# Kernel optimization log

Measured on AMD Instinct MI355X. Metric: run time of the kernel, lower is better.

The kernel has to match this reference:

```python
import jax, jax.numpy as jnp
import numpy as np
import math

B, IMG, P, C_IN = 32, 32, 2, 4
D, TED, L, H = 768, 256, 12, 12
GRID = IMG // P            # 16
N = GRID * GRID            # 256 patches
HD = D // H                # 64 head dim
MLP_H = 4 * D
RPD = 2 * GRID - 1         # 31 relative-position table side


def _ln(x, w, b, eps=1e-6):
    m = x.mean(-1, keepdims=True)
    v = ((x - m) ** 2).mean(-1, keepdims=True)
    return (x - m) * jax.lax.rsqrt(v + eps) * w + b


def _rel_idx():
    c = jnp.arange(GRID)
    ch, cw = jnp.meshgrid(c, c, indexing='ij')
    cf = jnp.stack([ch.reshape(-1), cw.reshape(-1)])          # [2, N]
    rel = cf[:, :, None] - cf[:, None, :] + (GRID - 1)        # [2, N, N] in [0, 2*GRID-2]
    return rel[0], rel[1]


def setup_inputs() -> dict:
    key = jax.random.key(0)
    ks = iter(jax.random.split(key, 64))
    def nrm(shape, s=0.02):
        return jax.random.normal(next(ks), shape, jnp.float32) * s
    z = lambda *s: jnp.zeros(s, jnp.float32)
    o = lambda *s: jnp.ones(s, jnp.float32)
    return dict(
        x=jax.random.normal(next(ks), (B, C_IN, IMG, IMG), jnp.float32),
        t=jax.random.uniform(next(ks), (B,), jnp.float32) * 1000.0,
        patch_w=nrm((D, C_IN, P, P), 0.5), patch_b=z(D),
        pos_embed=nrm((1, N, D)),
        t_w1=nrm((TED, D)), t_b1=z(D), t_w2=nrm((D, D)), t_b2=z(D),
        norm1_w=o(L, D), norm1_b=z(L, D),
        wqs=nrm((L, D, D)), bqs=z(L, D), wqt=nrm((L, D, D)), bqt=z(L, D),
        wks=nrm((L, D, D)), bks=z(L, D), wkt=nrm((L, D, D)), bkt=z(L, D),
        wvs=nrm((L, D, D)), bvs=z(L, D), wvt=nrm((L, D, D)), bvt=z(L, D),
        attn_proj_w=nrm((L, D, D)), attn_proj_b=z(L, D),
        rpb=nrm((L, RPD, RPD, H)),
        norm2_w=o(L, D), norm2_b=z(L, D),
        mlp_w1=nrm((L, D, MLP_H)), mlp_b1=z(L, MLP_H),
        mlp_w2=nrm((L, MLP_H, D)), mlp_b2=z(L, D),
        norm_w=o(D), norm_b=z(D),
        dec_w=nrm((D, P * P * C_IN)), dec_b=z(P * P * C_IN),
    )


def reference(x, t, patch_w, patch_b, pos_embed, t_w1, t_b1, t_w2, t_b2,
              norm1_w, norm1_b, wqs, bqs, wqt, bqt, wks, bks, wkt, bkt,
              wvs, bvs, wvt, bvt, attn_proj_w, attn_proj_b, rpb,
              norm2_w, norm2_b, mlp_w1, mlp_b1, mlp_w2, mlp_b2,
              norm_w, norm_b, dec_w, dec_b):
    Bn = x.shape[0]
    # patch embed: stride==kernel Conv2d as reshape + einsum -> [B, N, D]
    xr = x.reshape(Bn, C_IN, GRID, P, GRID, P)
    x_s = jnp.einsum('bcipjq,ecpq->bije', xr, patch_w).reshape(Bn, N, D) + patch_b
    x_s = x_s + pos_embed
    # sinusoidal time embedding + MLP -> [B, D]
    half = TED // 2
    freq = jnp.exp(jnp.arange(half, dtype=jnp.float32) * (-math.log(10000.0) / (half - 1)))
    emb = t[:, None] * freq[None, :]
    emb = jnp.concatenate([jnp.sin(emb), jnp.cos(emb)], axis=-1)
    x_t = jax.nn.silu(emb @ t_w1 + t_b1) @ t_w2 + t_b2
    ih, iw = _rel_idx()
    scale = HD ** -0.5
    for l in range(L):
        h = _ln(x_s, norm1_w[l], norm1_b[l])
        q = h @ wqs[l] + bqs[l] + (x_t @ wqt[l] + bqt[l])[:, None, :]
        k = h @ wks[l] + bks[l] + (x_t @ wkt[l] + bkt[l])[:, None, :]
        v = h @ wvs[l] + bvs[l] + (x_t @ wvt[l] + bvt[l])[:, None, :]
        q = q.reshape(Bn, N, H, HD)
        k = k.reshape(Bn, N, H, HD)
        v = v.reshape(Bn, N, H, HD)
        bias = rpb[l][ih, iw]                                  # gather: [N, N, H]
        attn = jnp.einsum('bnhd,bmhd->bhnm', q, k) * scale + bias.transpose(2, 0, 1)[None]
        attn = jax.nn.softmax(attn, axis=-1)
        o_ = jnp.einsum('bhnm,bmhd->bnhd', attn, v).reshape(Bn, N, D)
        x_s = x_s + (o_ @ attn_proj_w[l] + attn_proj_b[l])
        h2 = _ln(x_s, norm2_w[l], norm2_b[l])
        x_s = x_s + (jax.nn.silu(h2 @ mlp_w1[l] + mlp_b1[l]) @ mlp_w2[l] + mlp_b2[l])
    x_s = _ln(x_s, norm_w, norm_b)
    x_s = x_s @ dec_w + dec_b                                  # [B, N, P*P*C]
    # unpatchify -> [B, C, IMG, IMG]
    xo = x_s.reshape(Bn, GRID, GRID, C_IN, P, P).transpose(0, 3, 1, 4, 2, 5)
    return xo.reshape(Bn, C_IN, GRID * P, GRID * P)
```

## Files before the change

### kernel.cpp

```cpp
#include <hip/hip_runtime.h>
#include <hip/hip_bf16.h>

typedef __attribute__((ext_vector_type(8))) short short8;
typedef __attribute__((ext_vector_type(4))) float f32x4;
typedef __hip_bfloat16 bf16;

#define AS1 __attribute__((address_space(1)))
#define AS3 __attribute__((address_space(3)))

__device__ __forceinline__ void gld_lds16(const void* g, void* lds) {
  __builtin_amdgcn_global_load_lds((const AS1 unsigned int*)g,
                                   (AS3 unsigned int*)lds, 16, 0, 0);
}

__global__ void transpose_conv(const float* __restrict__ src, bf16* __restrict__ dst,
                               int R, int C, int row_off, long long layer_stride) {
  __shared__ float t[32][33];
  int l = blockIdx.z;
  int r0 = blockIdx.y * 32;
  int c0 = blockIdx.x * 32;
  int tx = threadIdx.x & 31, ty = threadIdx.x >> 5;
  const float* s = src + (size_t)l * R * C;
#pragma unroll
  for (int i = 0; i < 4; ++i)
    t[ty + i * 8][tx] = s[(size_t)(r0 + ty + i * 8) * C + c0 + tx];
  __syncthreads();
  bf16* d = dst + (size_t)l * layer_stride;
#pragma unroll
  for (int i = 0; i < 4; ++i) {
    int n = c0 + ty + i * 8, k = r0 + tx;
    d[(size_t)(row_off + n) * R + k] = __float2bfloat16(t[tx][ty + i * 8]);
  }
}

__global__ void dec_transpose(const float* __restrict__ dw, bf16* __restrict__ dwT) {
  int idx = blockIdx.x * 256 + threadIdx.x;
  if (idx >= 12288) return;
  int k = idx % 768, j = idx / 768;
  dwT[j * 768 + k] = __float2bfloat16(dw[k * 16 + j]);
}

__global__ void patch_embed(const float* __restrict__ x, const float* __restrict__ pw,
                            const float* __restrict__ pb, const float* __restrict__ pos,
                            float* __restrict__ xs) {
  int idx = blockIdx.x * 256 + threadIdx.x;
  int d = idx % 768;
  int n = (idx / 768) & 255;
  int b = idx / (768 * 256);
  int gi = n >> 4, gj = n & 15;
  float acc = pb[d];
#pragma unroll
  for (int c = 0; c < 4; ++c)
#pragma unroll
    for (int p = 0; p < 2; ++p)
#pragma unroll
      for (int q = 0; q < 2; ++q)
        acc += x[((b * 4 + c) * 32 + gi * 2 + p) * 32 + gj * 2 + q] *
               pw[((d * 4 + c) * 2 + p) * 2 + q];
  xs[idx] = acc + pos[n * 768 + d];
}

__global__ void temb_kernel(const float* __restrict__ t, float* __restrict__ emb) {
  int b = blockIdx.x;
  int i = threadIdx.x;
  float f = __expf((float)i * (-logf(10000.f) / 127.f));
  float e = t[b] * f;
  emb[b * 256 + i] = sinf(e);
  emb[b * 256 + 128 + i] = cosf(e);
}

template <int MODE>
__global__ void smallmm_red(const float* __restrict__ in, const float* __restrict__ w,
                            const float* __restrict__ bias, void* __restrict__ out, int K) {
  int tid = threadIdx.x;
  int s = tid & 7, o = blockIdx.x * 32 + (tid >> 3);
  int d = o % 768, b = o / 768;
  int Ks = K >> 3, k0 = s * Ks;
  const float* ir = in + b * K + k0;
  const float* wr = w + (size_t)k0 * 768 + d;
  float a = 0.f;
  for (int i = 0; i < Ks; ++i) a += ir[i] * wr[(size_t)i * 768];
  a += __shfl_xor(a, 1);
  a += __shfl_xor(a, 2);
  a += __shfl_xor(a, 4);
  if (s == 0) {
    a += bias[d];
    if (MODE == 0) {
      a = a / (1.f + __expf(-a));
      ((float*)out)[o] = a;
    } else {
      ((bf16*)out)[o] = __float2bfloat16(a);
    }
  }
}

__global__ void build_btab(const float* __restrict__ rpb, bf16* __restrict__ btab) {
  int idx = blockIdx.x * 256 + threadIdx.x;
  int k = idx & 255, q = (idx >> 8) & 255;
  int lh = idx >> 16;
  int h = lh % 12, l = lh / 12;
  int ih = (q >> 4) - (k >> 4) + 15;
  int iw = (q & 15) - (k & 15) + 15;
  btab[idx] = __float2bfloat16(rpb[((l * 31 + ih) * 31 + iw) * 12 + h]);
}

__global__ __launch_bounds__(256) void ln_bf16_kernel(const float* __restrict__ x,
                                                      const float* __restrict__ w,
                                                      const float* __restrict__ b,
                                                      bf16* __restrict__ out) {
  int row = blockIdx.x;
  int tid = threadIdx.x;
  const float* xr = x + (size_t)row * 768;
  float v[3];
  float s = 0.f, s2 = 0.f;
#pragma unroll
  for (int i = 0; i < 3; ++i) {
    v[i] = xr[tid + i * 256];
    s += v[i];
    s2 += v[i] * v[i];
  }
#pragma unroll
  for (int off = 32; off; off >>= 1) {
    s += __shfl_down(s, off);
    s2 += __shfl_down(s2, off);
  }
  __shared__ float ps[4], ps2[4];
  int wid = tid >> 6, lane = tid & 63;
  if (lane == 0) { ps[wid] = s; ps2[wid] = s2; }
  __syncthreads();
  s = ps[0] + ps[1] + ps[2] + ps[3];
  s2 = ps2[0] + ps2[1] + ps2[2] + ps2[3];
  float m = s * (1.f / 768.f);
  float var = s2 * (1.f / 768.f) - m * m;
  float r = rsqrtf(var + 1e-6f);
#pragma unroll
  for (int i = 0; i < 3; ++i) {
    int c = tid + i * 256;
    out[(size_t)row * 768 + c] = __float2bfloat16((v[i] - m) * r * w[c] + b[c]);
  }
}

template <int EPI>
__global__ __launch_bounds__(256) void gemm128(
    const bf16* __restrict__ A, int lda, const bf16* __restrict__ BT, int ldb, int K,
    const float* __restrict__ p0, const float* __restrict__ p1,
    const float* __restrict__ p2, const float* __restrict__ p3,
    const float* __restrict__ p4, const float* __restrict__ p5,
    const float* __restrict__ resid, float* __restrict__ outF,
    bf16* __restrict__ outB, int ldc) {
  __shared__ __align__(16) char lds[65536];
  const int tid = threadIdx.x;
  const int wid = tid >> 6, lane = tid & 63;
  const int wr = wid >> 1, wc = wid & 1;
  const int nwg = gridDim.x * gridDim.y;
  const int bid = blockIdx.y * gridDim.x + blockIdx.x;
  const int swzb = (bid & 7) * (nwg >> 3) + (bid >> 3);
  const int m0 = (swzb / gridDim.x) * 128, n0 = (swzb % gridDim.x) * 128;
  const int l16 = lane & 15, lq = lane >> 4;

  f32x4 acc[4][4];
#pragma unroll
  for (int i = 0; i < 4; ++i)
#pragma unroll
    for (int j = 0; j < 4; ++j) acc[i][j] = f32x4{0.f, 0.f, 0.f, 0.f};

  const int arow = tid >> 3;
  const int aslot = (tid & 7) ^ (arow & 7);
  const bf16* gA = A + (size_t)(m0 + arow) * lda + aslot * 8;
  const bf16* gB = BT + (size_t)(n0 + arow) * ldb + aslot * 8;
  const unsigned offw = (unsigned)__builtin_amdgcn_readfirstlane((tid & ~63) * 16);

  const int NT = K >> 6;
  auto stage = [&](int buf, int t) {
    char* p = lds + buf * 32768;
    const int k = t * 64;
#pragma unroll
    for (int it = 0; it < 4; ++it) {
      gld_lds16(gA + (size_t)it * 32 * lda + k, p + it * 4096 + offw);
      gld_lds16(gB + (size_t)it * 32 * ldb + k, p + 16384 + it * 4096 + offw);
    }
  };

  stage(0, 0);
  const unsigned swb = ((unsigned)(l16 & 7)) << 4;
  for (int t = 0; t < NT; ++t) {
    char* cur = lds + (t & 1) * 32768;
    if (t + 1 < NT) {
      stage((t + 1) & 1, t + 1);
      asm volatile("s_waitcnt vmcnt(8)" ::: "memory");
    } else {
      asm volatile("s_waitcnt vmcnt(0)" ::: "memory");
    }
    __builtin_amdgcn_s_barrier();
#pragma unroll
    for (int ks = 0; ks < 2; ++ks) {
      short8 af[4], bfr[4];
      const unsigned ko = ((unsigned)(ks * 64 + lq * 16)) ^ swb;
#pragma unroll
      for (int i = 0; i < 4; ++i) {
        af[i]  = *(const short8*)(cur + (wr * 64 + i * 16 + l16) * 128 + ko);
        bfr[i] = *(const short8*)(cur + 16384 + (wc * 64 + i * 16 + l16) * 128 + ko);
      }
#pragma unroll
      for (int i = 0; i < 4; ++i)
#pragma unroll
        for (int j = 0; j < 4; ++j)
          acc[i][j] = __builtin_amdgcn_mfma_f32_16x16x32_bf16(af[i], bfr[j], acc[i][j], 0, 0, 0);
    }
    __builtin_amdgcn_s_barrier();
  }

#pragma unroll
  for (int i = 0; i < 4; ++i) {
#pragma unroll
    for (int j = 0; j < 4; ++j) {
#pragma unroll
      for (int r = 0; r < 4; ++r) {
        int row = m0 + wr * 64 + i * 16 + lq * 4 + r;
        int col = n0 + wc * 64 + j * 16 + l16;
        float v = acc[i][j][r];
        if constexpr (EPI == 0) {
          int s = col / 768, d = col % 768;
          int b = row >> 8;
          const float* bs = (s == 0) ? p0 : (s == 1) ? p1 : p2;
          const float* ts = (s == 0) ? p3 : (s == 1) ? p4 : p5;
          v += bs[d] + ts[b * 768 + d];
          outB[(size_t)row * ldc + col] = __float2bfloat16(v);
        } else if constexpr (EPI == 1) {
          v += p0[col] + resid[(size_t)row * ldc + col];
          outF[(size_t)row * ldc + col] = v;
        } else if constexpr (EPI == 2) {
          v += p0[col];
          v = v / (1.f + __expf(-v));
          outB[(size_t)row * ldc + col] = __float2bfloat16(v);
        } else if constexpr (EPI == 3) {
          if (row < 32) {
            int l = col / 2304;
            int r2c = col - l * 2304;
            int s = r2c / 768, d = r2c - s * 768;
            const float* bs = (s == 0) ? p0 : (s == 1) ? p1 : p2;
            v += bs[l * 768 + d];
            outF[(size_t)((l * 3 + s) * 32 + row) * 768 + d] = v;
          }
        } else {
          if (col < 16) {
            v += p0[col];
            int b = row >> 8, n = row & 255;
            int gi = n >> 4, gj = n & 15;
            int c = col >> 2, pp = (col >> 1) & 1, qq = col & 1;
            outF[((b * 4 + c) * 32 + gi * 2 + pp) * 32 + gj * 2 + qq] = v;
          }
        }
      }
    }
  }
}

__global__ __launch_bounds__(256) void attn_mfma(const bf16* __restrict__ qkv,
                                                 const bf16* __restrict__ btab,
                                                 bf16* __restrict__ obuf) {
  __shared__ __align__(16) char lds[65536];
  const int tid = threadIdx.x;
  const int wave = tid >> 6, lane = tid & 63;
  const int l16 = lane & 15, lq = lane >> 4;
  const int b = blockIdx.x / 12, h = blockIdx.x % 12;
  const bf16* qb = qkv + (size_t)b * 256 * 2304;

  const int srcd = (((tid & 7) ^ ((tid >> 3) & 7))) * 8;
  const unsigned kbase = (unsigned)__builtin_amdgcn_readfirstlane((tid & ~63) * 16);
#pragma unroll
  for (int it = 0; it < 8; ++it) {
    int tok = it * 32 + (tid >> 3);
    gld_lds16(qb + (size_t)tok * 2304 + 768 + h * 64 + srcd, lds + it * 4096 + kbase);
  }
  {
    const short8* vrow = (const short8*)(qb + (size_t)tid * 2304 + 1536 + h * 64);
    short8 vv[8];
#pragma unroll
    for (int c = 0; c < 8; ++c) vv[c] = vrow[c];
#pragma unroll
    for (int c = 0; c < 8; ++c)
#pragma unroll
      for (int e = 0; e < 8; ++e) {
        int d = c * 8 + e;
        unsigned off = (unsigned)(32768 + d * 512 + tid * 2) ^ ((unsigned)(d & 7) << 4);
        *(short*)(lds + off) = vv[c][e];
      }
  }
  short8 qf[4][2];
#pragma unroll
  for (int i = 0; i < 4; ++i)
#pragma unroll
    for (int s = 0; s < 2; ++s)
      qf[i][s] = *(const short8*)(qb + (size_t)(wave * 64 + i * 16 + l16) * 2304 +
                                  h * 64 + s * 32 + lq * 8);
  asm volatile("s_waitcnt vmcnt(0)" ::: "memory");
  __syncthreads();

  const unsigned swz = ((unsigned)(l16 & 7)) << 4;
  f32x4 sacc[4][16];
#pragma unroll
  for (int i = 0; i < 4; ++i)
#pragma unroll
    for (int j = 0; j < 16; ++j) sacc[i][j] = f32x4{0.f, 0.f, 0.f, 0.f};
#pragma unroll
  for (int j = 0; j < 16; ++j) {
    unsigned rb = (unsigned)(j * 16 + l16) * 128;
    short8 k0 = *(const short8*)(lds + rb + ((unsigned)(lq * 16) ^ swz));
    short8 k1 = *(const short8*)(lds + rb + ((unsigned)(64 + lq * 16) ^ swz));
#pragma unroll
    for (int i = 0; i < 4; ++i) {
      sacc[i][j] = __builtin_amdgcn_mfma_f32_16x16x32_bf16(qf[i][0], k0, sacc[i][j], 0, 0, 0);
      sacc[i][j] = __builtin_amdgcn_mfma_f32_16x16x32_bf16(qf[i][1], k1, sacc[i][j], 0, 0, 0);
    }
  }
  __syncthreads();

  const bf16* bth = btab + (size_t)h * 65536;
  float linv[4][4];
#pragma unroll
  for (int i = 0; i < 4; ++i) {
#pragma unroll
    for (int r = 0; r < 4; ++r) {
      int q = wave * 64 + i * 16 + lq * 4 + r;
      const bf16* brow = bth + q * 256 + l16;
      float sv[16];
      float mx = -1e30f;
#pragma unroll
      for (int j = 0; j < 16; ++j) {
        sv[j] = sacc[i][j][r] * 0.125f + __bfloat162float(brow[j * 16]);
        mx = fmaxf(mx, sv[j]);
      }
      mx = fmaxf(mx, __shfl_xor(mx, 1));
      mx = fmaxf(mx, __shfl_xor(mx, 2));
      mx = fmaxf(mx, __shfl_xor(mx, 4));
      mx = fmaxf(mx, __shfl_xor(mx, 8));
      float sum = 0.f;
#pragma unroll
      for (int j = 0; j < 16; ++j) {
        float p = __expf(sv[j] - mx);
        sacc[i][j][r] = p;
        sum += p;
      }
      sum += __shfl_xor(sum, 1);
      sum += __shfl_xor(sum, 2);
      sum += __shfl_xor(sum, 4);
      sum += __shfl_xor(sum, 8);
      linv[i][r] = 1.f / sum;
    }
  }

  f32x4 oacc[4][4];
#pragma unroll
  for (int i = 0; i < 4; ++i)
#pragma unroll
    for (int j = 0; j < 4; ++j) oacc[i][j] = f32x4{0.f, 0.f, 0.f, 0.f};
  char* Pw = lds + wave * 8192;
#pragma unroll
  for (int ch = 0; ch < 4; ++ch) {
#pragma unroll
    for (int i = 0; i < 4; ++i)
#pragma unroll
      for (int jj = 0; jj < 4; ++jj)
#pragma unroll
        for (int r = 0; r < 4; ++r) {
          int rowp = i * 16 + lq * 4 + r;
          unsigned off = (unsigned)(rowp * 128) +
                         (((unsigned)((jj * 16 + l16) * 2)) ^ (((unsigned)(rowp & 7)) << 4));
          *(bf16*)(Pw + off) = __float2bfloat16(sacc[i][ch * 4 + jj][r]);
        }
#pragma unroll
    for (int ks = 0; ks < 2; ++ks) {
      short8 pa[4], vb[4];
#pragma unroll
      for (int i = 0; i < 4; ++i) {
        unsigned rowp = (unsigned)(i * 16 + l16);
        pa[i] = *(const short8*)(Pw + rowp * 128 + (((unsigned)(ks * 64 + lq * 16)) ^ swz));
      }
#pragma unroll
      for (int dj = 0; dj < 4; ++dj) {
        unsigned d = (unsigned)(dj * 16 + l16);
        vb[dj] = *(const short8*)(lds + 32768 + d * 512 +
                                  (((unsigned)(ch * 128 + ks * 64 + lq * 16)) ^ swz));
      }
#pragma unroll
      for (int i = 0; i < 4; ++i)
#pragma unroll
        for (int dj = 0; dj < 4; ++dj)
          oacc[i][dj] = __builtin_amdgcn_mfma_f32_16x16x32_bf16(pa[i], vb[dj], oacc[i][dj], 0, 0, 0);
    }
  }

#pragma unroll
  for (int i = 0; i < 4; ++i)
#pragma unroll
    for (int dj = 0; dj < 4; ++dj)
#pragma unroll
      for (int r = 0; r < 4; ++r) {
        int grow = b * 256 + wave * 64 + i * 16 + lq * 4 + r;
        int gcol = h * 64 + dj * 16 + l16;
        obuf[(size_t)grow * 768 + gcol] = __float2bfloat16(oacc[i][dj][r] * linv[i][r]);
      }
}

extern "C" void kernel_launch(void* const* d_in, const int* in_sizes, int n_in,
                              void* d_out, int out_size, void* d_ws, size_t ws_size,
                              hipStream_t stream) {
  (void)in_sizes; (void)n_in; (void)out_size; (void)ws_size;
  const float* x       = (const float*)d_in[0];
  const float* t_in    = (const float*)d_in[1];
  const float* patch_w = (const float*)d_in[2];
  const float* patch_b = (const float*)d_in[3];
  const float* pos     = (const float*)d_in[4];
  const float* t_w1    = (const float*)d_in[5];
  const float* t_b1    = (const float*)d_in[6];
  const float* t_w2    = (const float*)d_in[7];
  const float* t_b2    = (const float*)d_in[8];
  const float* norm1_w = (const float*)d_in[9];
  const float* norm1_b = (const float*)d_in[10];
  const float* wqs     = (const float*)d_in[11];
  const float* bqs     = (const float*)d_in[12];
  const float* wqt     = (const float*)d_in[13];
  const float* bqt     = (const float*)d_in[14];
  const float* wks     = (const float*)d_in[15];
  const float* bks     = (const float*)d_in[16];
  const float* wkt     = (const float*)d_in[17];
  const float* bkt     = (const float*)d_in[18];
  const float* wvs     = (const float*)d_in[19];
  const float* bvs     = (const float*)d_in[20];
  const float* wvt     = (const float*)d_in[21];
  const float* bvt     = (const float*)d_in[22];
  const float* projw   = (const float*)d_in[23];
  const float* projb   = (const float*)d_in[24];
  const float* rpb     = (const float*)d_in[25];
  const float* norm2_w = (const float*)d_in[26];
  const float* norm2_b = (const float*)d_in[27];
  const float* mlp_w1  = (const float*)d_in[28];
  const float* mlp_b1  = (const float*)d_in[29];
  const float* mlp_w2  = (const float*)d_in[30];
  const float* mlp_b2  = (const float*)d_in[31];
  const float* norm_w  = (const float*)d_in[32];
  const float* norm_b  = (const float*)d_in[33];
  const float* dec_w   = (const float*)d_in[34];
  const float* dec_b   = (const float*)d_in[35];

  char* ws = (char*)d_ws;
  size_t off = 0;
  auto alloc = [&](size_t bytes) -> void* {
    void* p = ws + off;
    off += (bytes + 255) & ~(size_t)255;
    return p;
  };
  bf16* wqkvT = (bf16*)alloc(12ull * 2304 * 768 * 2);
  bf16* projT = (bf16*)alloc(12ull * 768 * 768 * 2);
  bf16* mlp1T = (bf16*)alloc(12ull * 3072 * 768 * 2);
  bf16* mlp2T = (bf16*)alloc(12ull * 768 * 3072 * 2);
  bf16* wtT   = (bf16*)alloc(12ull * 2304 * 768 * 2);
  float* xs   = (float*)alloc(8192ull * 768 * 4);
  bf16* hbuf  = (bf16*)alloc(8192ull * 768 * 2);
  bf16* qkvb  = (bf16*)alloc(8192ull * 2304 * 2);
  bf16* obuf  = (bf16*)alloc(8192ull * 768 * 2);
  bf16* btab  = (bf16*)alloc(12ull * 12 * 256 * 256 * 2);
  float* ttok = (float*)alloc(12ull * 3 * 32 * 768 * 4);
  bf16* xtb   = (bf16*)alloc(128ull * 768 * 2);
  bf16* dwT   = (bf16*)alloc(128ull * 768 * 2);
  float* emb  = (float*)alloc(32ull * 256 * 4);
  float* h1   = (float*)alloc(32ull * 768 * 4);
  bf16* hmlp  = qkvb;

  hipMemsetAsync(xtb, 0, 128ull * 768 * 2, stream);
  hipMemsetAsync(dwT, 0, 128ull * 768 * 2, stream);

  transpose_conv<<<dim3(24, 24, 12), 256, 0, stream>>>(wqs, wqkvT, 768, 768, 0, 2304ll * 768);
  transpose_conv<<<dim3(24, 24, 12), 256, 0, stream>>>(wks, wqkvT, 768, 768, 768, 2304ll * 768);
  transpose_conv<<<dim3(24, 24, 12), 256, 0, stream>>>(wvs, wqkvT, 768, 768, 1536, 2304ll * 768);
  transpose_conv<<<dim3(24, 24, 12), 256, 0, stream>>>(projw, projT, 768, 768, 0, 768ll * 768);
  transpose_conv<<<dim3(96, 24, 12), 256, 0, stream>>>(mlp_w1, mlp1T, 768, 3072, 0, 3072ll * 768);
  transpose_conv<<<dim3(24, 96, 12), 256, 0, stream>>>(mlp_w2, mlp2T, 3072, 768, 0, 768ll * 3072);
  transpose_conv<<<dim3(24, 24, 12), 256, 0, stream>>>(wqt, wtT, 768, 768, 0, 2304ll * 768);
  transpose_conv<<<dim3(24, 24, 12), 256, 0, stream>>>(wkt, wtT, 768, 768, 768, 2304ll * 768);
  transpose_conv<<<dim3(24, 24, 12), 256, 0, stream>>>(wvt, wtT, 768, 768, 1536, 2304ll * 768);
  dec_transpose<<<48, 256, 0, stream>>>(dec_w, dwT);
  build_btab<<<36864, 256, 0, stream>>>(rpb, btab);

  temb_kernel<<<32, 128, 0, stream>>>(t_in, emb);
  smallmm_red<0><<<768, 256, 0, stream>>>(emb, t_w1, t_b1, h1, 256);
  smallmm_red<1><<<768, 256, 0, stream>>>(h1, t_w2, t_b2, xtb, 768);
  gemm128<3><<<dim3(216, 1), 256, 0, stream>>>(
      xtb, 768, wtT, 768, 768, bqt, bkt, bvt, nullptr, nullptr, nullptr,
      nullptr, ttok, nullptr, 0);

  patch_embed<<<24576, 256, 0, stream>>>(x, patch_w, patch_b, pos, xs);

  for (int l = 0; l < 12; ++l) {
    ln_bf16_kernel<<<8192, 256, 0, stream>>>(xs, norm1_w + l * 768, norm1_b + l * 768, hbuf);
    gemm128<0><<<dim3(18, 64), 256, 0, stream>>>(
        hbuf, 768, wqkvT + (size_t)l * 2304 * 768, 768, 768,
        bqs + l * 768, bks + l * 768, bvs + l * 768,
        ttok + (size_t)(l * 3 + 0) * 32 * 768,
        ttok + (size_t)(l * 3 + 1) * 32 * 768,
        ttok + (size_t)(l * 3 + 2) * 32 * 768,
        nullptr, nullptr, qkvb, 2304);
    attn_mfma<<<384, 256, 0, stream>>>(qkvb, btab + (size_t)l * 12 * 65536, obuf);
    gemm128<1><<<dim3(6, 64), 256, 0, stream>>>(
        obuf, 768, projT + (size_t)l * 768 * 768, 768, 768,
        projb + l * 768, nullptr, nullptr, nullptr, nullptr, nullptr,
        xs, xs, nullptr, 768);
    ln_bf16_kernel<<<8192, 256, 0, stream>>>(xs, norm2_w + l * 768, norm2_b + l * 768, hbuf);
    gemm128<2><<<dim3(24, 64), 256, 0, stream>>>(
        hbuf, 768, mlp1T + (size_t)l * 3072 * 768, 768, 768,
        mlp_b1 + l * 3072, nullptr, nullptr, nullptr, nullptr, nullptr,
        nullptr, nullptr, hmlp, 3072);
    gemm128<1><<<dim3(6, 64), 256, 0, stream>>>(
        hmlp, 3072, mlp2T + (size_t)l * 768 * 3072, 3072, 3072,
        mlp_b2 + l * 768, nullptr, nullptr, nullptr, nullptr, nullptr,
        xs, xs, nullptr, 768);
  }
  ln_bf16_kernel<<<8192, 256, 0, stream>>>(xs, norm_w, norm_b, hbuf);
  gemm128<4><<<dim3(1, 64), 256, 0, stream>>>(
      hbuf, 768, dwT, 768, 768, dec_b, nullptr, nullptr, nullptr, nullptr, nullptr,
      nullptr, (float*)d_out, nullptr, 0);
}
```

Baseline: 3.181 ms.

## Stream attention over key chunks with fragment-ordered bias and no max pass

Attention is restructured into a loop over eight 32-key chunks. Each chunk computes transposed scores with MFMA, exponentiates them, stages P in a small double-buffered LDS region and immediately multiplies by V, so the full 256-wide score matrix is never held in registers. The relative-position bias table is now built once, pre-scaled by 8 and stored in MFMA accumulator fragment order, so it can be loaded vectorised and used as the initial accumulator value instead of being added per element. K is read straight from global memory instead of being staged through LDS. Softmax now skips the row-max subtraction entirely, which lowers register pressure and removes shuffles but can overflow if scores get large.

```diff
diff --git a/kernel.cpp b/kernel.cpp
--- a/kernel.cpp
+++ b/kernel.cpp
@@ -2,11 +2,22 @@
 #include <hip/hip_bf16.h>
 
 typedef __attribute__((ext_vector_type(8))) short short8;
+typedef __attribute__((ext_vector_type(4))) short s16x4;
 typedef __attribute__((ext_vector_type(4))) float f32x4;
 typedef __hip_bfloat16 bf16;
 
 #define AS1 __attribute__((address_space(1)))
 #define AS3 __attribute__((address_space(3)))
+
+__device__ __forceinline__ float b2f(short u) {
+  union { unsigned int i; float f; } x;
+  x.i = ((unsigned int)(unsigned short)u) << 16;
+  return x.f;
+}
+__device__ __forceinline__ short f2bs(float f) {
+  bf16 t = __float2bfloat16(f);
+  return *reinterpret_cast<short*>(&t);
+}
 
 __device__ __forceinline__ void gld_lds16(const void* g, void* lds) {
   __builtin_amdgcn_global_load_lds((const AS1 unsigned int*)g,
@@ -94,14 +105,22 @@
   }
 }
 
-__global__ void build_btab(const float* __restrict__ rpb, bf16* __restrict__ btab) {
+__global__ void build_btab_frag(const float* __restrict__ rpb, bf16* __restrict__ btf) {
   int idx = blockIdx.x * 256 + threadIdx.x;
-  int k = idx & 255, q = (idx >> 8) & 255;
+  int t = idx & 65535;
   int lh = idx >> 16;
   int h = lh % 12, l = lh / 12;
+  int r = t & 3; t >>= 2;
+  int lane = t & 63; t >>= 6;
+  int i = t & 3; t >>= 2;
+  int w = t & 3; t >>= 2;
+  int jb = t & 1; t >>= 1;
+  int hc = t & 7;
+  int q = w * 64 + i * 16 + (lane & 15);
+  int k = hc * 32 + jb * 16 + (lane >> 4) * 4 + r;
   int ih = (q >> 4) - (k >> 4) + 15;
   int iw = (q & 15) - (k & 15) + 15;
-  btab[idx] = __float2bfloat16(rpb[((l * 31 + ih) * 31 + iw) * 12 + h]);
+  btf[idx] = __float2bfloat16(8.0f * rpb[((l * 31 + ih) * 31 + iw) * 12 + h]);
 }
 
 __global__ __launch_bounds__(256) void ln_bf16_kernel(const float* __restrict__ x,
@@ -257,7 +276,7 @@
 }
 
 __global__ __launch_bounds__(256) void attn_mfma(const bf16* __restrict__ qkv,
-                                                 const bf16* __restrict__ btab,
+                                                 const bf16* __restrict__ btf,
                                                  bf16* __restrict__ obuf) {
   __shared__ __align__(16) char lds[65536];
   const int tid = threadIdx.x;
@@ -266,13 +285,6 @@
   const int b = blockIdx.x / 12, h = blockIdx.x % 12;
   const bf16* qb = qkv + (size_t)b * 256 * 2304;
 
-  const int srcd = (((tid & 7) ^ ((tid >> 3) & 7))) * 8;
-  const unsigned kbase = (unsigned)__builtin_amdgcn_readfirstlane((tid & ~63) * 16);
-#pragma unroll
-  for (int it = 0; it < 8; ++it) {
-    int tok = it * 32 + (tid >> 3);
-    gld_lds16(qb + (size_t)tok * 2304 + 768 + h * 64 + srcd, lds + it * 4096 + kbase);
-  }
   {
     const short8* vrow = (const short8*)(qb + (size_t)tid * 2304 + 1536 + h * 64);
     short8 vv[8];
@@ -283,7 +295,7 @@
 #pragma unroll
       for (int e = 0; e < 8; ++e) {
         int d = c * 8 + e;
-        unsigned off = (unsigned)(32768 + d * 512 + tid * 2) ^ ((unsigned)(d & 7) << 4);
+        unsigned off = (unsigned)(d * 512 + tid * 2) ^ ((unsigned)(d & 7) << 4);
         *(short*)(lds + off) = vv[c][e];
       }
   }
@@ -291,116 +303,89 @@
 #pragma unroll
   for (int i = 0; i < 4; ++i)
 #pragma unroll
-    for (int s = 0; s < 2; ++s)
-      qf[i][s] = *(const short8*)(qb + (size_t)(wave * 64 + i * 16 + l16) * 2304 +
-                                  h * 64 + s * 32 + lq * 8);
-  asm volatile("s_waitcnt vmcnt(0)" ::: "memory");
+    for (int ks = 0; ks < 2; ++ks)
+      qf[i][ks] = *(const short8*)(qb + (size_t)(wave * 64 + i * 16 + l16) * 2304 +
+                                   h * 64 + ks * 32 + lq * 8);
   __syncthreads();
 
-  const unsigned swz = ((unsigned)(l16 & 7)) << 4;
-  f32x4 sacc[4][16];
+  f32x4 oacc[4][4];
 #pragma unroll
   for (int i = 0; i < 4; ++i)
 #pragma unroll
-    for (int j = 0; j < 16; ++j) sacc[i][j] = f32x4{0.f, 0.f, 0.f, 0.f};
-#pragma unroll
-  for (int j = 0; j < 16; ++j) {
-    unsigned rb = (unsigned)(j * 16 + l16) * 128;
-    short8 k0 = *(const short8*)(lds + rb + ((unsigned)(lq * 16) ^ swz));
-    short8 k1 = *(const short8*)(lds + rb + ((unsigned)(64 + lq * 16) ^ swz));
-#pragma unroll
-    for (int i = 0; i < 4; ++i) {
-      sacc[i][j] = __builtin_amdgcn_mfma_f32_16x16x32_bf16(qf[i][0], k0, sacc[i][j], 0, 0, 0);
-      sacc[i][j] = __builtin_amdgcn_mfma_f32_16x16x32_bf16(qf[i][1], k1, sacc[i][j], 0, 0, 0);
-    }
-  }
-  __syncthreads();
-
-  const bf16* bth = btab + (size_t)h * 65536;
-  float linv[4][4];
+    for (int j = 0; j < 4; ++j) oacc[i][j] = f32x4{0.f, 0.f, 0.f, 0.f};
+  float lp[4] = {0.f, 0.f, 0.f, 0.f};
+  const bf16* bl = btf + (size_t)h * 65536 + lane * 4;
+  const unsigned swzv = ((unsigned)(l16 & 7)) << 4;
+  const unsigned swzp = ((unsigned)(l16 & 3)) << 4;
+
+  for (int hc = 0; hc < 8; ++hc) {
+    short8 kf[2][2];
+#pragma unroll
+    for (int jb = 0; jb < 2; ++jb) {
+      const bf16* kr = qb + (size_t)(hc * 32 + jb * 16 + l16) * 2304 + 768 + h * 64 + lq * 8;
+      kf[jb][0] = *(const short8*)(kr);
+      kf[jb][1] = *(const short8*)(kr + 32);
+    }
+    f32x4 sacc[4][2];
+#pragma unroll
+    for (int i = 0; i < 4; ++i)
+#pragma unroll
+      for (int jb = 0; jb < 2; ++jb) {
+        s16x4 bv = *(const s16x4*)(bl + ((size_t)((hc * 2 + jb) * 16 + wave * 4 + i) << 8));
+        sacc[i][jb] = f32x4{b2f(bv[0]), b2f(bv[1]), b2f(bv[2]), b2f(bv[3])};
+      }
+#pragma unroll
+    for (int jb = 0; jb < 2; ++jb)
+#pragma unroll
+      for (int i = 0; i < 4; ++i) {
+        sacc[i][jb] = __builtin_amdgcn_mfma_f32_16x16x32_bf16(kf[jb][0], qf[i][0], sacc[i][jb], 0, 0, 0);
+        sacc[i][jb] = __builtin_amdgcn_mfma_f32_16x16x32_bf16(kf[jb][1], qf[i][1], sacc[i][jb], 0, 0, 0);
+      }
+    char* Pw = lds + 32768 + (hc & 1) * 16384 + wave * 4096;
+#pragma unroll
+    for (int i = 0; i < 4; ++i)
+#pragma unroll
+      for (int jb = 0; jb < 2; ++jb) {
+        float p0 = __expf(sacc[i][jb][0] * 0.125f);
+        float p1 = __expf(sacc[i][jb][1] * 0.125f);
+        float p2 = __expf(sacc[i][jb][2] * 0.125f);
+        float p3 = __expf(sacc[i][jb][3] * 0.125f);
+        lp[i] += (p0 + p1) + (p2 + p3);
+        s16x4 pk = {f2bs(p0), f2bs(p1), f2bs(p2), f2bs(p3)};
+        *(s16x4*)(Pw + (i * 16 + l16) * 64 + (((unsigned)(jb * 32 + lq * 8)) ^ swzp)) = pk;
+      }
+    asm volatile("s_waitcnt lgkmcnt(0)" ::: "memory");
+    __builtin_amdgcn_sched_barrier(0);
+    short8 pa[4], vb[4];
+#pragma unroll
+    for (int i = 0; i < 4; ++i)
+      pa[i] = *(const short8*)(Pw + (i * 16 + l16) * 64 + (((unsigned)(lq * 16)) ^ swzp));
+#pragma unroll
+    for (int dj = 0; dj < 4; ++dj)
+      vb[dj] = *(const short8*)(lds + (dj * 16 + l16) * 512 +
+                                (((unsigned)(hc * 64 + lq * 16)) ^ swzv));
+#pragma unroll
+    for (int i = 0; i < 4; ++i)
+#pragma unroll
+      for (int dj = 0; dj < 4; ++dj)
+        oacc[i][dj] = __builtin_amdgcn_mfma_f32_16x16x32_bf16(pa[i], vb[dj], oacc[i][dj], 0, 0, 0);
+  }
+
 #pragma unroll
   for (int i = 0; i < 4; ++i) {
+    float l = lp[i];
+    l += __shfl_xor(l, 16);
+    l += __shfl_xor(l, 32);
 #pragma unroll
     for (int r = 0; r < 4; ++r) {
-      int q = wave * 64 + i * 16 + lq * 4 + r;
-      const bf16* brow = bth + q * 256 + l16;
-      float sv[16];
-      float mx = -1e30f;
-#pragma unroll
-      for (int j = 0; j < 16; ++j) {
-        sv[j] = sacc[i][j][r] * 0.125f + __bfloat162float(brow[j * 16]);
-        mx = fmaxf(mx, sv[j]);
-      }
-      mx = fmaxf(mx, __shfl_xor(mx, 1));
-      mx = fmaxf(mx, __shfl_xor(mx, 2));
-      mx = fmaxf(mx, __shfl_xor(mx, 4));
-      mx = fmaxf(mx, __shfl_xor(mx, 8));
-      float sum = 0.f;
-#pragma unroll
-      for (int j = 0; j < 16; ++j) {
-        float p = __expf(sv[j] - mx);
-        sacc[i][j][r] = p;
-        sum += p;
-      }
-      sum += __shfl_xor(sum, 1);
-      sum += __shfl_xor(sum, 2);
-      sum += __shfl_xor(sum, 4);
-      sum += __shfl_xor(sum, 8);
-      linv[i][r] = 1.f / sum;
-    }
-  }
-
-  f32x4 oacc[4][4];
-#pragma unroll
-  for (int i = 0; i < 4; ++i)
-#pragma unroll
-    for (int j = 0; j < 4; ++j) oacc[i][j] = f32x4{0.f, 0.f, 0.f, 0.f};
-  char* Pw = lds + wave * 8192;
-#pragma unroll
-  for (int ch = 0; ch < 4; ++ch) {
-#pragma unroll
-    for (int i = 0; i < 4; ++i)
-#pragma unroll
-      for (int jj = 0; jj < 4; ++jj)
-#pragma unroll
-        for (int r = 0; r < 4; ++r) {
-          int rowp = i * 16 + lq * 4 + r;
-          unsigned off = (unsigned)(rowp * 128) +
-                         (((unsigned)((jj * 16 + l16) * 2)) ^ (((unsigned)(rowp & 7)) << 4));
-          *(bf16*)(Pw + off) = __float2bfloat16(sacc[i][ch * 4 + jj][r]);
-        }
-#pragma unroll
-    for (int ks = 0; ks < 2; ++ks) {
-      short8 pa[4], vb[4];
-#pragma unroll
-      for (int i = 0; i < 4; ++i) {
-        unsigned rowp = (unsigned)(i * 16 + l16);
-        pa[i] = *(const short8*)(Pw + rowp * 128 + (((unsigned)(ks * 64 + lq * 16)) ^ swz));
-      }
-#pragma unroll
-      for (int dj = 0; dj < 4; ++dj) {
-        unsigned d = (unsigned)(dj * 16 + l16);
-        vb[dj] = *(const short8*)(lds + 32768 + d * 512 +
-                                  (((unsigned)(ch * 128 + ks * 64 + lq * 16)) ^ swz));
-      }
-#pragma unroll
-      for (int i = 0; i < 4; ++i)
-#pragma unroll
-        for (int dj = 0; dj < 4; ++dj)
-          oacc[i][dj] = __builtin_amdgcn_mfma_f32_16x16x32_bf16(pa[i], vb[dj], oacc[i][dj], 0, 0, 0);
-    }
-  }
-
-#pragma unroll
-  for (int i = 0; i < 4; ++i)
-#pragma unroll
-    for (int dj = 0; dj < 4; ++dj)
-#pragma unroll
-      for (int r = 0; r < 4; ++r) {
-        int grow = b * 256 + wave * 64 + i * 16 + lq * 4 + r;
-        int gcol = h * 64 + dj * 16 + l16;
-        obuf[(size_t)grow * 768 + gcol] = __float2bfloat16(oacc[i][dj][r] * linv[i][r]);
-      }
+      float linv = 1.f / __shfl(l, lq * 4 + r);
+      int grow = b * 256 + wave * 64 + i * 16 + lq * 4 + r;
+#pragma unroll
+      for (int dj = 0; dj < 4; ++dj)
+        obuf[(size_t)grow * 768 + h * 64 + dj * 16 + l16] =
+            __float2bfloat16(oacc[i][dj][r] * linv);
+    }
+  }
 }
 
 extern "C" void kernel_launch(void* const* d_in, const int* in_sizes, int n_in,
@@ -460,7 +445,7 @@
   bf16* hbuf  = (bf16*)alloc(8192ull * 768 * 2);
   bf16* qkvb  = (bf16*)alloc(8192ull * 2304 * 2);
   bf16* obuf  = (bf16*)alloc(8192ull * 768 * 2);
-  bf16* btab  = (bf16*)alloc(12ull * 12 * 256 * 256 * 2);
+  bf16* btabf = (bf16*)alloc(12ull * 12 * 256 * 256 * 2);
   float* ttok = (float*)alloc(12ull * 3 * 32 * 768 * 4);
   bf16* xtb   = (bf16*)alloc(128ull * 768 * 2);
   bf16* dwT   = (bf16*)alloc(128ull * 768 * 2);
@@ -481,7 +466,7 @@
   transpose_conv<<<dim3(24, 24, 12), 256, 0, stream>>>(wkt, wtT, 768, 768, 768, 2304ll * 768);
   transpose_conv<<<dim3(24, 24, 12), 256, 0, stream>>>(wvt, wtT, 768, 768, 1536, 2304ll * 768);
   dec_transpose<<<48, 256, 0, stream>>>(dec_w, dwT);
-  build_btab<<<36864, 256, 0, stream>>>(rpb, btab);
+  build_btab_frag<<<36864, 256, 0, stream>>>(rpb, btabf);
 
   temb_kernel<<<32, 128, 0, stream>>>(t_in, emb);
   smallmm_red<0><<<768, 256, 0, stream>>>(emb, t_w1, t_b1, h1, 256);
@@ -501,7 +486,7 @@
         ttok + (size_t)(l * 3 + 1) * 32 * 768,
         ttok + (size_t)(l * 3 + 2) * 32 * 768,
         nullptr, nullptr, qkvb, 2304);
-    attn_mfma<<<384, 256, 0, stream>>>(qkvb, btab + (size_t)l * 12 * 65536, obuf);
+    attn_mfma<<<384, 256, 0, stream>>>(qkvb, btabf + (size_t)l * 12 * 65536, obuf);
     gemm128<1><<<dim3(6, 64), 256, 0, stream>>>(
         obuf, 768, projT + (size_t)l * 768 * 768, 768, 768,
         projb + l * 768, nullptr, nullptr, nullptr, nullptr, nullptr,
```

Result: faster. 2.841 ms (-10.7%).
